# Optimization experiments

Hardware: AMD Instinct MI355X
Metric: run time of the kernel (lower is better)

## Reference

```python
import jax, jax.numpy as jnp
import numpy as np

N = 50000      # nodes
E = 800000     # edges (before self-loops)
IN = 128       # in_channels
C = 64         # hidden_channels (per head)
H = 2          # heads
OUT = 40       # out_channels (classes)
SLOPE = 0.2    # PyG GATConv leaky_relu negative_slope


def setup_inputs() -> dict:
    key = jax.random.key(0)
    ks = jax.random.split(key, 12)
    def glorot(k, shape, fan):
        return (jax.random.normal(k, shape, jnp.float32) / np.float32(np.sqrt(fan)))
    x = jax.random.normal(ks[0], (N, IN), jnp.float32)
    edge_index = jax.random.randint(ks[1], (2, E), 0, N, dtype=jnp.int32)
    return {
        "x": x,
        "edge_index": edge_index,
        "W0": glorot(ks[2], (IN, H * C), IN),
        "a_src0": glorot(ks[3], (H, C), C),
        "a_dst0": glorot(ks[4], (H, C), C),
        "b0": jnp.zeros((H * C,), jnp.float32),
        "W1": glorot(ks[5], (H * C, H * C), H * C),
        "a_src1": glorot(ks[6], (H, C), C),
        "a_dst1": glorot(ks[7], (H, C), C),
        "b1": jnp.zeros((H * C,), jnp.float32),
        "lin_w": glorot(ks[8], (H * C * 2, OUT), H * C * 2),
        "lin_b": jnp.zeros((OUT,), jnp.float32),
    }


def gat_conv(x, W, a_src, a_dst, b, src, dst):
    # x: [N, F_in] -> h: [N, H, C]
    h = (x @ W).reshape(-1, H, C)
    # per-node attention logits (PyG splits a into src/dst halves)
    es = jnp.einsum("nhc,hc->nh", h, a_src)  # [N, H]
    ed = jnp.einsum("nhc,hc->nh", h, a_dst)  # [N, H]
    e = jax.nn.leaky_relu(es[src] + ed[dst], SLOPE)  # [Etot, H]
    # segment softmax over incoming edges of each destination node
    m = jax.ops.segment_max(e, dst, num_segments=N)          # [N, H]
    m = jnp.where(jnp.isneginf(m), 0.0, m)
    w = jnp.exp(e - m[dst])                                  # [Etot, H]
    denom = jax.ops.segment_sum(w, dst, num_segments=N)      # [N, H]
    alpha = w / jnp.maximum(denom[dst], 1e-16)               # [Etot, H]
    # scatter-aggregate messages: [Etot, H, C] -> [N, H, C]
    out = jax.ops.segment_sum(alpha[:, :, None] * h[src], dst, num_segments=N)
    return out.reshape(-1, H * C) + b  # concat=True over heads


def reference(x, edge_index, W0, a_src0, a_dst0, b0, W1, a_src1, a_dst1, b1, lin_w, lin_b):
    # PyG GATConv adds self-loops by default
    loops = jnp.arange(N, dtype=edge_index.dtype)
    src = jnp.concatenate([edge_index[0], loops])
    dst = jnp.concatenate([edge_index[1], loops])
    h1 = jax.nn.elu(gat_conv(x, W0, a_src0, a_dst0, b0, src, dst))   # [N, H*C]
    h2 = jax.nn.elu(gat_conv(h1, W1, a_src1, a_dst1, b1, src, dst))  # [N, H*C]
    h_cat = jnp.concatenate([h1, h2], axis=1)                        # [N, 2*H*C]
    logits = h_cat @ lin_w + lin_b                                   # [N, OUT]
    return jax.nn.log_softmax(logits, axis=1)
```

## Files before the change

### kernel.cpp

```cpp
#include <hip/hip_runtime.h>
#include <hip/hip_fp16.h>
#include <math.h>

#define NN 50000
#define E0 800000
#define ET 850000
#define NBK 196
#define TILE 4096
#define NTILES 208
#define CAP 8192

typedef unsigned int uint32;
typedef unsigned short u16;
typedef __attribute__((ext_vector_type(8))) _Float16 f16x8;
typedef __attribute__((ext_vector_type(4))) float f32x4;

__device__ __forceinline__ u16 f2h(float f) {
  return __half_as_ushort(__float2half(f));
}
__device__ __forceinline__ float h2f(u16 u) {
  return __half2float(__ushort_as_half(u));
}

__device__ __forceinline__ int block_incl_scan(int v, int tid, int* wsum) {
  const int lane = tid & 63, wid = tid >> 6;
  int val = v;
#pragma unroll
  for (int off = 1; off < 64; off <<= 1) {
    int t = __shfl_up(val, off);
    if (lane >= off) val += t;
  }
  if (lane == 63) wsum[wid] = val;
  __syncthreads();
  int wofs = 0;
#pragma unroll
  for (int w = 0; w < 4; ++w) wofs += (w < wid) ? wsum[w] : 0;
  return val + wofs;
}

__global__ __launch_bounds__(256) void partition_prep_kernel(
    const int* __restrict__ ei, int* __restrict__ gcursor, uint32* __restrict__ packed,
    const float* __restrict__ W0, const float* __restrict__ W1,
    const float* __restrict__ lw,
    u16* __restrict__ w0t, u16* __restrict__ w1t, u16* __restrict__ lwt)
{
  __shared__ __align__(16) char smem[23872];
  const int b = blockIdx.x;
  const int tid = threadIdx.x;
  if (b < NTILES) {
    int* hist  = (int*)smem;
    int* scanb = (int*)(smem + 1024);
    int* gofs  = (int*)(smem + 2048);
    int* wsum  = (int*)(smem + 3072);
    uint32* shuf = (uint32*)(smem + 3088);
    unsigned char* sbkt = (unsigned char*)(smem + 19472);
    const int t0 = b * TILE;
    hist[tid] = 0;
    __syncthreads();
    int myb[16]; int myr[16]; uint32 mypk[16];
#pragma unroll
    for (int it = 0; it < 4; ++it) {
      const int q = it * 256 + tid;
      const int e4 = t0 + q * 4;
      const bool valid = (e4 < ET);
      int sa[4], da[4];
      if (valid) {
        if (e4 + 3 < E0) {
          int4 sv = *(const int4*)&ei[e4];
          int4 dv = *(const int4*)&ei[E0 + e4];
          sa[0] = sv.x; sa[1] = sv.y; sa[2] = sv.z; sa[3] = sv.w;
          da[0] = dv.x; da[1] = dv.y; da[2] = dv.z; da[3] = dv.w;
        } else {
#pragma unroll
          for (int u = 0; u < 4; ++u) { sa[u] = e4 - E0 + u; da[u] = sa[u]; }
        }
      }
#pragma unroll
      for (int u = 0; u < 4; ++u) {
        const int i = it * 4 + u;
        myb[i] = -1;
        if (valid) {
          const int src = sa[u], dst = da[u];
          myb[i] = dst >> 8;
          mypk[i] = ((uint32)(dst & 255) << 16) | (uint32)src;
          myr[i] = atomicAdd(&hist[myb[i]], 1);
        }
      }
    }
    __syncthreads();
    const int v = (tid < NBK) ? hist[tid] : 0;
    const int incl = block_incl_scan(v, tid, wsum);
    if (tid < NBK) {
      scanb[tid] = incl - v;
      gofs[tid] = (v > 0) ? atomicAdd(&gcursor[tid], v) : 0;
    }
    __syncthreads();
#pragma unroll
    for (int i = 0; i < 16; ++i) {
      if (myb[i] >= 0) {
        int slot = scanb[myb[i]] + myr[i];
        shuf[slot] = mypk[i];
        sbkt[slot] = (unsigned char)myb[i];
      }
    }
    __syncthreads();
    const int tcount = (t0 + TILE <= ET) ? TILE : (ET - t0);
    for (int i = tid; i < tcount; i += 256) {
      int bb = sbkt[i];
      packed[(size_t)bb * CAP + gofs[bb] + (i - scanb[bb])] = shuf[i];
    }
  } else if (b < NTILES + 2) {
    const float* W = (b == NTILES) ? W0 : W1;
    u16* Wt = (b == NTILES) ? w0t : w1t;
    float (*tile)[129] = (float(*)[129])smem;
    for (int k0 = 0; k0 < 128; k0 += 32) {
      __syncthreads();
#pragma unroll
      for (int it = 0; it < 4; ++it) {
        int q = tid + it * 256;
        int kk = q >> 5, n4 = (q & 31) * 4;
        float4 v = *(const float4*)&W[(k0 + kk) * 128 + n4];
        tile[kk][n4 + 0] = v.x; tile[kk][n4 + 1] = v.y;
        tile[kk][n4 + 2] = v.z; tile[kk][n4 + 3] = v.w;
      }
      __syncthreads();
      int n = tid >> 1, h = (tid & 1) * 16;
      __align__(16) u16 tmp[16];
#pragma unroll
      for (int j = 0; j < 16; ++j) tmp[j] = f2h(tile[h + j][n]);
      *(uint4*)&Wt[n * 128 + k0 + h] = *(uint4*)&tmp[0];
      *(uint4*)&Wt[n * 128 + k0 + h + 8] = *(uint4*)&tmp[8];
    }
  } else {
    for (int idx = tid; idx < 48 * 256; idx += 256) {
      int j = idx >> 8, k = idx & 255;
      lwt[idx] = (j < 40) ? f2h(lw[k * 40 + j]) : (u16)0;
    }
  }
}

__device__ __forceinline__ void build_body(
    char* smem, int b,
    const uint32* __restrict__ packed, const int* __restrict__ gcursor,
    int2* __restrict__ rowinfo, u16* __restrict__ csr_src)
{
  int* h      = (int*)smem;
  int* sc     = (int*)(smem + 1024);
  int* cur    = (int*)(smem + 2048);
  int* wsum   = (int*)(smem + 3072);
  int* ptot_p = (int*)(smem + 3088);
  u16* simg   = (u16*)(smem + 3104);
  const int tid = threadIdx.x;
  const int cnt = gcursor[b];
  const uint32* pk = packed + (size_t)b * CAP;
  h[tid] = 0;
  cur[tid] = 0;
  __syncthreads();
  for (int i = tid; i < cnt; i += 256) atomicAdd(&h[(pk[i] >> 16) & 255], 1);
  __syncthreads();
  const int pd = (h[tid] + 7) & ~7;
  const int incl = block_incl_scan(pd, tid, wsum);
  sc[tid] = incl - pd;
  if (tid == 255) *ptot_p = incl;
  __syncthreads();
  const int ptot = *ptot_p;
  for (int i = tid; i < ptot; i += 256) simg[i] = (u16)NN;
  __syncthreads();
  for (int i = tid; i < cnt; i += 256) {
    uint32 p = pk[i];
    int dl = (p >> 16) & 255;
    int r = atomicAdd(&cur[dl], 1);
    simg[sc[dl] + r] = (u16)(p & 0xFFFFu);
  }
  __syncthreads();
  int n = b * 256 + tid;
  if (n < NN) rowinfo[n] = make_int2(b * CAP + sc[tid], pd);
  uint32* dst = (uint32*)(csr_src + (size_t)b * CAP);
  const uint32* sim32 = (const uint32*)simg;
  for (int i = tid; i < (ptot >> 1); i += 256) dst[i] = sim32[i];
}

__global__ __launch_bounds__(256) void gemm_att_kernel(
    const float* __restrict__ Xf, const u16* __restrict__ Xh,
    const u16* __restrict__ Wt,
    const float* __restrict__ avs, const float* __restrict__ avd,
    u16* __restrict__ hfeat, float* __restrict__ es, float* __restrict__ ed,
    int nnodes,
    const uint32* __restrict__ packed, const int* __restrict__ gcursor,
    int2* __restrict__ rowinfo, u16* __restrict__ csr_src)
{
  __shared__ __align__(16) char smem[20608];
  const int ngemm = (nnodes + 63) >> 6;
  if ((int)blockIdx.x >= ngemm) {
    build_body(smem, (int)blockIdx.x - ngemm, packed, gcursor, rowinfo, csr_src);
    return;
  }
  u16* hout   = (u16*)smem;
  float* es_s = (float*)(smem + 17408);
  float* ed_s = (float*)(smem + 17920);
  const int tid = threadIdx.x;
  const int wid = tid >> 6, lane = tid & 63;
  const int quad = lane >> 4, lc = lane & 15;
  const int n0 = blockIdx.x * 64;
  if (blockIdx.x == 0 && tid < 2) es[2 * NN + tid] = -1e30f;

  const int arow = wid * 16 + lc;
  const int rrow = min(n0 + arow, nnodes - 1);

  f32x4 acc[8];
#pragma unroll
  for (int t = 0; t < 8; ++t) acc[t] = (f32x4){0.f, 0.f, 0.f, 0.f};
#pragma unroll
  for (int ks = 0; ks < 4; ++ks) {
    const int k0 = ks * 32 + quad * 8;
    f16x8 a;
    if (Xf) {
      const float4* xr = (const float4*)&Xf[(size_t)rrow * 128 + k0];
      float4 v0 = xr[0], v1 = xr[1];
      a[0] = (_Float16)v0.x; a[1] = (_Float16)v0.y;
      a[2] = (_Float16)v0.z; a[3] = (_Float16)v0.w;
      a[4] = (_Float16)v1.x; a[5] = (_Float16)v1.y;
      a[6] = (_Float16)v1.z; a[7] = (_Float16)v1.w;
    } else {
      a = *(const f16x8*)&Xh[(size_t)rrow * 128 + k0];
    }
#pragma unroll
    for (int t = 0; t < 8; ++t) {
      f16x8 bfr = *(const f16x8*)&Wt[(t * 16 + lc) * 128 + k0];
      acc[t] = __builtin_amdgcn_mfma_f32_16x16x32_f16(a, bfr, acc[t], 0, 0, 0);
    }
  }

  float av_s[8], av_d[8];
#pragma unroll
  for (int t = 0; t < 8; ++t) { av_s[t] = avs[t * 16 + lc]; av_d[t] = avd[t * 16 + lc]; }
#pragma unroll
  for (int r = 0; r < 4; ++r) {
    float s0 = 0.f, s1 = 0.f, d0 = 0.f, d1 = 0.f;
#pragma unroll
    for (int t = 0; t < 4; ++t) { s0 += acc[t][r] * av_s[t]; d0 += acc[t][r] * av_d[t]; }
#pragma unroll
    for (int t = 4; t < 8; ++t) { s1 += acc[t][r] * av_s[t]; d1 += acc[t][r] * av_d[t]; }
#pragma unroll
    for (int m = 1; m < 16; m <<= 1) {
      s0 += __shfl_xor(s0, m); s1 += __shfl_xor(s1, m);
      d0 += __shfl_xor(d0, m); d1 += __shfl_xor(d1, m);
    }
    if (lc == 0) {
      int row = wid * 16 + quad * 4 + r;
      es_s[row] = s0; es_s[64 + row] = s1;
      ed_s[row] = d0; ed_s[64 + row] = d1;
    }
  }
#pragma unroll
  for (int t = 0; t < 8; ++t)
#pragma unroll
    for (int r = 0; r < 4; ++r)
      hout[(wid * 16 + quad * 4 + r) * 136 + t * 16 + lc] = f2h(acc[t][r]);
  __syncthreads();
#pragma unroll
  for (int it = 0; it < 4; ++it) {
    int g = tid + it * 256;
    int r = g >> 4, c8 = (g & 15) * 8;
    if (n0 + r < nnodes)
      *(uint4*)&hfeat[(size_t)(n0 + r) * 128 + c8] = *(const uint4*)&hout[r * 136 + c8];
  }
  if (tid < 64) {
    int n = n0 + tid;
    if (n < nnodes) {
      es[n * 2 + 0] = es_s[tid];      es[n * 2 + 1] = es_s[64 + tid];
      ed[n * 2 + 0] = ed_s[tid];      ed[n * 2 + 1] = ed_s[64 + tid];
    }
  }
}

__global__ __launch_bounds__(256) void aggregate_kernel(
    const uint4* __restrict__ hfeat4, const float* __restrict__ es, const float* __restrict__ ed,
    const int2* __restrict__ rowinfo, const u16* __restrict__ csr_src,
    const float* __restrict__ bias, u16* __restrict__ out, int nnodes)
{
  int n = (blockIdx.x * blockDim.x + threadIdx.x) >> 6;
  int lane = threadIdx.x & 63;
  if (n >= nnodes) return;
  const int eg = lane >> 4;
  const int fl = lane & 15;
  const int hd = (fl >= 8) ? 1 : 0;
  const int2 ri = rowinfo[n];
  const int nch = ri.y >> 3;
  const int j0 = ri.x + eg;
  const float edn = ed[n * 2 + hd];

  float acc[8];
#pragma unroll
  for (int t = 0; t < 8; ++t) acc[t] = 0.f;
  float den = 0.f;

  int iA0 = csr_src[j0], iA1 = csr_src[j0 + 4];
  float e0 = es[iA0 * 2 + hd] + edn; e0 = fmaxf(e0, 0.2f * e0);
  float e1 = es[iA1 * 2 + hd] + edn; e1 = fmaxf(e1, 0.2f * e1);
  float wA0 = __expf(e0), wA1 = __expf(e1);
  uint4 hA0 = hfeat4[(size_t)iA0 * 16 + fl];
  uint4 hA1 = hfeat4[(size_t)iA1 * 16 + fl];

  for (int c = 0;;) {
    const bool more = (c + 1 < nch);
    float wB0 = 0.f, wB1 = 0.f; uint4 hB0, hB1;
    if (more) {
      const int jb = j0 + (c + 1) * 8;
      int iB0 = csr_src[jb], iB1 = csr_src[jb + 4];
      float f0 = es[iB0 * 2 + hd] + edn; f0 = fmaxf(f0, 0.2f * f0);
      float f1 = es[iB1 * 2 + hd] + edn; f1 = fmaxf(f1, 0.2f * f1);
      wB0 = __expf(f0); wB1 = __expf(f1);
      hB0 = hfeat4[(size_t)iB0 * 16 + fl];
      hB1 = hfeat4[(size_t)iB1 * 16 + fl];
    }
    acc[0] = fmaf(wA0, h2f((u16)(hA0.x & 0xFFFFu)), acc[0]);
    acc[1] = fmaf(wA0, h2f((u16)(hA0.x >> 16)),     acc[1]);
    acc[2] = fmaf(wA0, h2f((u16)(hA0.y & 0xFFFFu)), acc[2]);
    acc[3] = fmaf(wA0, h2f((u16)(hA0.y >> 16)),     acc[3]);
    acc[4] = fmaf(wA0, h2f((u16)(hA0.z & 0xFFFFu)), acc[4]);
    acc[5] = fmaf(wA0, h2f((u16)(hA0.z >> 16)),     acc[5]);
    acc[6] = fmaf(wA0, h2f((u16)(hA0.w & 0xFFFFu)), acc[6]);
    acc[7] = fmaf(wA0, h2f((u16)(hA0.w >> 16)),     acc[7]);
    acc[0] = fmaf(wA1, h2f((u16)(hA1.x & 0xFFFFu)), acc[0]);
    acc[1] = fmaf(wA1, h2f((u16)(hA1.x >> 16)),     acc[1]);
    acc[2] = fmaf(wA1, h2f((u16)(hA1.y & 0xFFFFu)), acc[2]);
    acc[3] = fmaf(wA1, h2f((u16)(hA1.y >> 16)),     acc[3]);
    acc[4] = fmaf(wA1, h2f((u16)(hA1.z & 0xFFFFu)), acc[4]);
    acc[5] = fmaf(wA1, h2f((u16)(hA1.z >> 16)),     acc[5]);
    acc[6] = fmaf(wA1, h2f((u16)(hA1.w & 0xFFFFu)), acc[6]);
    acc[7] = fmaf(wA1, h2f((u16)(hA1.w >> 16)),     acc[7]);
    den += wA0 + wA1;
    if (!more) break;
    wA0 = wB0; wA1 = wB1; hA0 = hB0; hA1 = hB1;
    ++c;
  }

#pragma unroll
  for (int t = 0; t < 8; ++t) {
    acc[t] += __shfl_xor(acc[t], 16);
    acc[t] += __shfl_xor(acc[t], 32);
  }
  den += __shfl_xor(den, 16);
  den += __shfl_xor(den, 32);

  if (eg == 0) {
    float inv = 1.f / den;
    float4 b0 = *(const float4*)&bias[fl * 8];
    float4 b1 = *(const float4*)&bias[fl * 8 + 4];
    float bv[8] = {b0.x, b0.y, b0.z, b0.w, b1.x, b1.y, b1.z, b1.w};
    u16 pk[8];
#pragma unroll
    for (int t = 0; t < 8; ++t) {
      float v = acc[t] * inv + bv[t];
      v = (v > 0.f) ? v : (__expf(v) - 1.f);
      pk[t] = f2h(v);
    }
    uint4 o;
    o.x = (uint32)pk[0] | ((uint32)pk[1] << 16);
    o.y = (uint32)pk[2] | ((uint32)pk[3] << 16);
    o.z = (uint32)pk[4] | ((uint32)pk[5] << 16);
    o.w = (uint32)pk[6] | ((uint32)pk[7] << 16);
    ((uint4*)out)[(size_t)n * 16 + fl] = o;
  }
}

__global__ __launch_bounds__(256) void final_kernel(
    const u16* __restrict__ h1b, const u16* __restrict__ h2b,
    const u16* __restrict__ lwt, const float* __restrict__ lb,
    float* __restrict__ out, int nnodes)
{
  const int tid = threadIdx.x;
  const int wid = tid >> 6, lane = tid & 63;
  const int quad = lane >> 4, lc = lane & 15;
  const int n0 = blockIdx.x * 64;
  const int arow = wid * 16 + lc;
  const int rrow = min(n0 + arow, nnodes - 1);

  f32x4 acc[3];
#pragma unroll
  for (int t = 0; t < 3; ++t) acc[t] = (f32x4){0.f, 0.f, 0.f, 0.f};
#pragma unroll
  for (int ks = 0; ks < 8; ++ks) {
    const u16* hsrc = (ks < 4) ? h1b : h2b;
    const int k0 = (ks & 3) * 32 + quad * 8;
    const int kl = ks * 32 + quad * 8;
    f16x8 a = *(const f16x8*)&hsrc[(size_t)rrow * 128 + k0];
#pragma unroll
    for (int t = 0; t < 3; ++t) {
      f16x8 b = *(const f16x8*)&lwt[(t * 16 + lc) * 256 + kl];
      acc[t] = __builtin_amdgcn_mfma_f32_16x16x32_f16(a, b, acc[t], 0, 0, 0);
    }
  }

  float bv[3];
  bool valid[3];
#pragma unroll
  for (int t = 0; t < 3; ++t) {
    int col = t * 16 + lc;
    valid[t] = (col < 40);
    bv[t] = valid[t] ? lb[col] : 0.f;
  }
#pragma unroll
  for (int r = 0; r < 4; ++r) {
    int row = wid * 16 + quad * 4 + r;
    int n = n0 + row;
    float v[3];
    float mx = -INFINITY;
#pragma unroll
    for (int t = 0; t < 3; ++t) {
      v[t] = acc[t][r] + bv[t];
      if (valid[t]) mx = fmaxf(mx, v[t]);
    }
    mx = fmaxf(mx, __shfl_xor(mx, 1));
    mx = fmaxf(mx, __shfl_xor(mx, 2));
    mx = fmaxf(mx, __shfl_xor(mx, 4));
    mx = fmaxf(mx, __shfl_xor(mx, 8));
    float s = 0.f;
#pragma unroll
    for (int t = 0; t < 3; ++t) if (valid[t]) s += __expf(v[t] - mx);
    s += __shfl_xor(s, 1);
    s += __shfl_xor(s, 2);
    s += __shfl_xor(s, 4);
    s += __shfl_xor(s, 8);
    float lg = mx + __logf(s);
    if (n < nnodes) {
#pragma unroll
      for (int t = 0; t < 3; ++t)
        if (valid[t]) out[(size_t)n * 40 + t * 16 + lc] = v[t] - lg;
    }
  }
}


extern "C" void kernel_launch(void* const* d_in, const int* in_sizes, int n_in,
                              void* d_out, int out_size, void* d_ws, size_t ws_size,
                              hipStream_t stream) {
  const float* x   = (const float*)d_in[0];
  const int*   ei  = (const int*)d_in[1];
  const float* W0  = (const float*)d_in[2];
  const float* as0 = (const float*)d_in[3];
  const float* ad0 = (const float*)d_in[4];
  const float* b0  = (const float*)d_in[5];
  const float* W1  = (const float*)d_in[6];
  const float* as1 = (const float*)d_in[7];
  const float* ad1 = (const float*)d_in[8];
  const float* b1  = (const float*)d_in[9];
  const float* lw  = (const float*)d_in[10];
  const float* lb  = (const float*)d_in[11];
  float* out = (float*)d_out;

  char* p = (char*)d_ws;
  auto carve = [&](size_t bytes) { char* r = p; p += (bytes + 255) & ~(size_t)255; return r; };
  u16* w0t    = (u16*)carve(128 * 128 * 2);
  u16* w1t    = (u16*)carve(128 * 128 * 2);
  u16* lwt    = (u16*)carve(48 * 256 * 2);
  u16* hfeat  = (u16*)carve((size_t)(NN + 1) * 128 * 2);
  u16* h1b    = (u16*)carve((size_t)NN * 128 * 2);
  u16* h2b    = (u16*)carve((size_t)NN * 128 * 2);
  float* es   = (float*)carve((size_t)(NN + 1) * 2 * 4);
  float* ed   = (float*)carve((size_t)NN * 2 * 4);
  int2* rowinfo = (int2*)carve((size_t)NN * 8);
  u16* csr    = (u16*)carve((size_t)NBK * CAP * 2);
  uint32* packed = (uint32*)carve((size_t)NBK * CAP * 4);
  int* gcursor = (int*)carve(NBK * 4);

  hipMemsetAsync(gcursor, 0, NBK * 4, stream);

  const int NG = (NN + 63) / 64;

  partition_prep_kernel<<<NTILES + 3, 256, 0, stream>>>(
      ei, gcursor, packed, W0, W1, lw, w0t, w1t, lwt);

  gemm_att_kernel<<<NG + NBK, 256, 0, stream>>>(
      x, nullptr, w0t, as0, ad0, hfeat, es, ed, NN, packed, gcursor, rowinfo, csr);
  aggregate_kernel<<<(NN * 64 + 255) / 256, 256, 0, stream>>>(
      (const uint4*)hfeat, es, ed, rowinfo, csr, b0, h1b, NN);

  gemm_att_kernel<<<NG, 256, 0, stream>>>(
      nullptr, h1b, w1t, as1, ad1, hfeat, es, ed, NN, packed, gcursor, rowinfo, csr);
  aggregate_kernel<<<(NN * 64 + 255) / 256, 256, 0, stream>>>(
      (const uint4*)hfeat, es, ed, rowinfo, csr, b1, h2b, NN);

  final_kernel<<<NG, 256, 0, stream>>>(h1b, h2b, lwt, lb, out, NN);
}
```

Before: 232.4 us.

## Fuse final linear and log-softmax into second aggregation kernel

Removes the separate final MFMA kernel and the h2 intermediate buffer by computing the 256->40 linear layer and log_softmax directly in the epilogue of the layer-2 aggregation. Each 64-lane wave holds one node's h1 and h2 slices, does scalar FMA dot products against the transposed weights, and reduces with cross-lane shuffles. This saves one launch and a full write and read of h2, but puts 40x256 scalar FMAs per node, plus many shuffles, on the already memory-bound gather kernel instead of using matrix cores.

New measurement: 243.0 us. 4.6% more time.

```diff
diff --git a/kernel.cpp b/kernel.cpp
--- a/kernel.cpp
+++ b/kernel.cpp
@@ -274,10 +274,13 @@
   }
 }
 
+template <bool HEAD>
 __global__ __launch_bounds__(256) void aggregate_kernel(
     const uint4* __restrict__ hfeat4, const float* __restrict__ es, const float* __restrict__ ed,
     const int2* __restrict__ rowinfo, const u16* __restrict__ csr_src,
-    const float* __restrict__ bias, u16* __restrict__ out, int nnodes)
+    const float* __restrict__ bias, u16* __restrict__ out, int nnodes,
+    const uint4* __restrict__ h1b4, const u16* __restrict__ lwt,
+    const float* __restrict__ lb, float* __restrict__ logits)
 {
   int n = (blockIdx.x * blockDim.x + threadIdx.x) >> 6;
   int lane = threadIdx.x & 63;
@@ -344,91 +347,76 @@
   den += __shfl_xor(den, 16);
   den += __shfl_xor(den, 32);
 
-  if (eg == 0) {
-    float inv = 1.f / den;
-    float4 b0 = *(const float4*)&bias[fl * 8];
-    float4 b1 = *(const float4*)&bias[fl * 8 + 4];
-    float bv[8] = {b0.x, b0.y, b0.z, b0.w, b1.x, b1.y, b1.z, b1.w};
-    u16 pk[8];
-#pragma unroll
-    for (int t = 0; t < 8; ++t) {
-      float v = acc[t] * inv + bv[t];
-      v = (v > 0.f) ? v : (__expf(v) - 1.f);
-      pk[t] = f2h(v);
-    }
-    uint4 o;
-    o.x = (uint32)pk[0] | ((uint32)pk[1] << 16);
-    o.y = (uint32)pk[2] | ((uint32)pk[3] << 16);
-    o.z = (uint32)pk[4] | ((uint32)pk[5] << 16);
-    o.w = (uint32)pk[6] | ((uint32)pk[7] << 16);
-    ((uint4*)out)[(size_t)n * 16 + fl] = o;
-  }
-}
-
-__global__ __launch_bounds__(256) void final_kernel(
-    const u16* __restrict__ h1b, const u16* __restrict__ h2b,
-    const u16* __restrict__ lwt, const float* __restrict__ lb,
-    float* __restrict__ out, int nnodes)
-{
-  const int tid = threadIdx.x;
-  const int wid = tid >> 6, lane = tid & 63;
-  const int quad = lane >> 4, lc = lane & 15;
-  const int n0 = blockIdx.x * 64;
-  const int arow = wid * 16 + lc;
-  const int rrow = min(n0 + arow, nnodes - 1);
-
-  f32x4 acc[3];
-#pragma unroll
-  for (int t = 0; t < 3; ++t) acc[t] = (f32x4){0.f, 0.f, 0.f, 0.f};
-#pragma unroll
-  for (int ks = 0; ks < 8; ++ks) {
-    const u16* hsrc = (ks < 4) ? h1b : h2b;
-    const int k0 = (ks & 3) * 32 + quad * 8;
-    const int kl = ks * 32 + quad * 8;
-    f16x8 a = *(const f16x8*)&hsrc[(size_t)rrow * 128 + k0];
-#pragma unroll
-    for (int t = 0; t < 3; ++t) {
-      f16x8 b = *(const f16x8*)&lwt[(t * 16 + lc) * 256 + kl];
-      acc[t] = __builtin_amdgcn_mfma_f32_16x16x32_f16(a, b, acc[t], 0, 0, 0);
-    }
-  }
-
-  float bv[3];
-  bool valid[3];
-#pragma unroll
-  for (int t = 0; t < 3; ++t) {
-    int col = t * 16 + lc;
-    valid[t] = (col < 40);
-    bv[t] = valid[t] ? lb[col] : 0.f;
-  }
-#pragma unroll
-  for (int r = 0; r < 4; ++r) {
-    int row = wid * 16 + quad * 4 + r;
-    int n = n0 + row;
-    float v[3];
-    float mx = -INFINITY;
-#pragma unroll
-    for (int t = 0; t < 3; ++t) {
-      v[t] = acc[t][r] + bv[t];
-      if (valid[t]) mx = fmaxf(mx, v[t]);
-    }
-    mx = fmaxf(mx, __shfl_xor(mx, 1));
-    mx = fmaxf(mx, __shfl_xor(mx, 2));
-    mx = fmaxf(mx, __shfl_xor(mx, 4));
-    mx = fmaxf(mx, __shfl_xor(mx, 8));
-    float s = 0.f;
-#pragma unroll
-    for (int t = 0; t < 3; ++t) if (valid[t]) s += __expf(v[t] - mx);
-    s += __shfl_xor(s, 1);
-    s += __shfl_xor(s, 2);
-    s += __shfl_xor(s, 4);
-    s += __shfl_xor(s, 8);
-    float lg = mx + __logf(s);
-    if (n < nnodes) {
-#pragma unroll
-      for (int t = 0; t < 3; ++t)
-        if (valid[t]) out[(size_t)n * 40 + t * 16 + lc] = v[t] - lg;
-    }
+  float inv = 1.f / den;
+  float4 b0 = *(const float4*)&bias[fl * 8];
+  float4 b1 = *(const float4*)&bias[fl * 8 + 4];
+  float bv[8] = {b0.x, b0.y, b0.z, b0.w, b1.x, b1.y, b1.z, b1.w};
+  u16 pk[8];
+#pragma unroll
+  for (int t = 0; t < 8; ++t) {
+    float v = acc[t] * inv + bv[t];
+    v = (v > 0.f) ? v : (__expf(v) - 1.f);
+    pk[t] = f2h(v);
+  }
+
+  if (!HEAD) {
+    if (eg == 0) {
+      uint4 o;
+      o.x = (uint32)pk[0] | ((uint32)pk[1] << 16);
+      o.y = (uint32)pk[2] | ((uint32)pk[3] << 16);
+      o.z = (uint32)pk[4] | ((uint32)pk[5] << 16);
+      o.w = (uint32)pk[6] | ((uint32)pk[7] << 16);
+      ((uint4*)out)[(size_t)n * 16 + fl] = o;
+    }
+    return;
+  }
+
+  float h2v[8], h1v[8];
+#pragma unroll
+  for (int t = 0; t < 8; ++t) h2v[t] = h2f(pk[t]);
+  {
+    uint4 h1r = h1b4[(size_t)n * 16 + fl];
+    h1v[0] = h2f((u16)(h1r.x & 0xFFFFu)); h1v[1] = h2f((u16)(h1r.x >> 16));
+    h1v[2] = h2f((u16)(h1r.y & 0xFFFFu)); h1v[3] = h2f((u16)(h1r.y >> 16));
+    h1v[4] = h2f((u16)(h1r.z & 0xFFFFu)); h1v[5] = h2f((u16)(h1r.z >> 16));
+    h1v[6] = h2f((u16)(h1r.w & 0xFFFFu)); h1v[7] = h2f((u16)(h1r.w >> 16));
+  }
+  float lg[10];
+#pragma unroll
+  for (int jj = 0; jj < 10; ++jj) {
+    const int j = eg * 10 + jj;
+    const f16x8 wa = *(const f16x8*)&lwt[j * 256 + fl * 8];
+    const f16x8 wb = *(const f16x8*)&lwt[j * 256 + 128 + fl * 8];
+    float p = 0.f;
+#pragma unroll
+    for (int t = 0; t < 8; ++t) p = fmaf(h1v[t], (float)wa[t], p);
+#pragma unroll
+    for (int t = 0; t < 8; ++t) p = fmaf(h2v[t], (float)wb[t], p);
+    lg[jj] = p;
+  }
+#pragma unroll
+  for (int m = 1; m < 16; m <<= 1)
+#pragma unroll
+    for (int jj = 0; jj < 10; ++jj) lg[jj] += __shfl_xor(lg[jj], m);
+  float mx = -INFINITY;
+#pragma unroll
+  for (int jj = 0; jj < 10; ++jj) {
+    lg[jj] += lb[eg * 10 + jj];
+    mx = fmaxf(mx, lg[jj]);
+  }
+  mx = fmaxf(mx, __shfl_xor(mx, 16));
+  mx = fmaxf(mx, __shfl_xor(mx, 32));
+  float s = 0.f;
+#pragma unroll
+  for (int jj = 0; jj < 10; ++jj) s += __expf(lg[jj] - mx);
+  s += __shfl_xor(s, 16);
+  s += __shfl_xor(s, 32);
+  const float lgs = mx + __logf(s);
+  if (fl < 10) {
+    float wv = lg[0];
+#pragma unroll
+    for (int jj = 1; jj < 10; ++jj) wv = (fl == jj) ? lg[jj] : wv;
+    logits[(size_t)n * 40 + eg * 10 + fl] = wv - lgs;
   }
 }
 
@@ -457,7 +445,6 @@
   u16* lwt    = (u16*)carve(48 * 256 * 2);
   u16* hfeat  = (u16*)carve((size_t)(NN + 1) * 128 * 2);
   u16* h1b    = (u16*)carve((size_t)NN * 128 * 2);
-  u16* h2b    = (u16*)carve((size_t)NN * 128 * 2);
   float* es   = (float*)carve((size_t)(NN + 1) * 2 * 4);
   float* ed   = (float*)carve((size_t)NN * 2 * 4);
   int2* rowinfo = (int2*)carve((size_t)NN * 8);
@@ -474,13 +461,13 @@
 
   gemm_att_kernel<<<NG + NBK, 256, 0, stream>>>(
       x, nullptr, w0t, as0, ad0, hfeat, es, ed, NN, packed, gcursor, rowinfo, csr);
-  aggregate_kernel<<<(NN * 64 + 255) / 256, 256, 0, stream>>>(
-      (const uint4*)hfeat, es, ed, rowinfo, csr, b0, h1b, NN);
+  aggregate_kernel<false><<<(NN * 64 + 255) / 256, 256, 0, stream>>>(
+      (const uint4*)hfeat, es, ed, rowinfo, csr, b0, h1b, NN,
+      nullptr, nullptr, nullptr, nullptr);
 
   gemm_att_kernel<<<NG, 256, 0, stream>>>(
       nullptr, h1b, w1t, as1, ad1, hfeat, es, ed, NN, packed, gcursor, rowinfo, csr);
-  aggregate_kernel<<<(NN * 64 + 255) / 256, 256, 0, stream>>>(
-      (const uint4*)hfeat, es, ed, rowinfo, csr, b1, h2b, NN);
-
-  final_kernel<<<NG, 256, 0, stream>>>(h1b, h2b, lwt, lb, out, NN);
-}
+  aggregate_kernel<true><<<(NN * 64 + 255) / 256, 256, 0, stream>>>(
+      (const uint4*)hfeat, es, ed, rowinfo, csr, b1, nullptr, NN,
+      (const uint4*)h1b, lwt, lb, out);
+}
```
